# Kernel optimization log

Hardware: AMD Instinct MI355X
Metric: run time of the kernel (lower is better)

## Reference

```python
import jax, jax.numpy as jnp
import numpy as np

B, H, W, C = 16, 56, 56, 384
HEADS, WIN, SHIFT = 12, 7, 3
HD = C // HEADS
HIDDEN = 4 * C
NWH, NWW = H // WIN, W // WIN
NW = NWH * NWW
WA = WIN * WIN  # 49 tokens per window


def _rel_pos_index():
    coords = np.stack(np.meshgrid(np.arange(WIN), np.arange(WIN), indexing='ij')).reshape(2, -1)
    rel = coords[:, :, None] - coords[:, None, :]          # [2, WA, WA]
    rel = rel.transpose(1, 2, 0)
    rel[:, :, 0] += WIN - 1
    rel[:, :, 1] += WIN - 1
    rel[:, :, 0] *= 2 * WIN - 1
    return rel.sum(-1)                                      # [WA, WA]


def _attn_mask():
    img = np.zeros((H, W))
    cnt = 0
    for hs in (slice(0, -WIN), slice(-WIN, -SHIFT), slice(-SHIFT, None)):
        for ws in (slice(0, -WIN), slice(-WIN, -SHIFT), slice(-SHIFT, None)):
            img[hs, ws] = cnt
            cnt += 1
    mw = img.reshape(NWH, WIN, NWW, WIN).transpose(0, 2, 1, 3).reshape(NW, WA)
    diff = mw[:, None, :] - mw[:, :, None]
    return np.where(diff != 0, -100.0, 0.0).astype(np.float32)  # [NW, WA, WA]


REL_IDX = jnp.asarray(_rel_pos_index())
MASK = jnp.asarray(_attn_mask())


def _ln(x, g, b):
    m = x.mean(-1, keepdims=True)
    v = ((x - m) ** 2).mean(-1, keepdims=True)
    return (x - m) / jnp.sqrt(v + 1e-5) * g + b


def setup_inputs() -> dict:
    key = jax.random.key(0)
    ks = jax.random.split(key, 6)
    s = 0.02
    return {
        'x': jax.random.normal(ks[0], (B, H, W, C), jnp.float32),
        'norm1_g': jnp.ones((C,), jnp.float32),
        'norm1_b': jnp.zeros((C,), jnp.float32),
        'qkv_w': jax.random.normal(ks[1], (C, 3 * C), jnp.float32) * s,
        'qkv_b': jnp.zeros((3 * C,), jnp.float32),
        'rel_bias': jax.random.normal(ks[2], ((2 * WIN - 1) ** 2, HEADS), jnp.float32) * s,
        'proj_w': jax.random.normal(ks[3], (C, C), jnp.float32) * s,
        'proj_b': jnp.zeros((C,), jnp.float32),
        'norm2_g': jnp.ones((C,), jnp.float32),
        'norm2_b': jnp.zeros((C,), jnp.float32),
        'fc1_w': jax.random.normal(ks[4], (C, HIDDEN), jnp.float32) * s,
        'fc1_b': jnp.zeros((HIDDEN,), jnp.float32),
        'fc2_w': jax.random.normal(ks[5], (HIDDEN, C), jnp.float32) * s,
        'fc2_b': jnp.zeros((C,), jnp.float32),
    }


def reference(x, norm1_g, norm1_b, qkv_w, qkv_b, rel_bias, proj_w, proj_b,
              norm2_g, norm2_b, fc1_w, fc1_b, fc2_w, fc2_b):
    # ---- shifted-window attention branch ----
    xs = _ln(x, norm1_g, norm1_b)
    xs = jnp.roll(xs, (-SHIFT, -SHIFT), axis=(1, 2))
    # window partition: [B,H,W,C] -> [B*NW, WA, C]
    xw = xs.reshape(B, NWH, WIN, NWW, WIN, C).transpose(0, 1, 3, 2, 4, 5).reshape(B * NW, WA, C)
    qkv = (xw @ qkv_w + qkv_b).reshape(B * NW, WA, 3, HEADS, HD)
    q = qkv[:, :, 0].transpose(0, 2, 1, 3)  # [bw, heads, WA, HD]
    k = qkv[:, :, 1].transpose(0, 2, 1, 3)
    v = qkv[:, :, 2].transpose(0, 2, 1, 3)
    attn = jnp.einsum('bhqd,bhkd->bhqk', q, k) * (HD ** -0.5)
    bias = rel_bias[REL_IDX].transpose(2, 0, 1)  # [heads, WA, WA]
    attn = attn + bias[None]
    attn = attn.reshape(B, NW, HEADS, WA, WA) + MASK[None, :, None]
    attn = jax.nn.softmax(attn, axis=-1).reshape(B * NW, HEADS, WA, WA)
    out = jnp.einsum('bhqk,bhkd->bhqd', attn, v).transpose(0, 2, 1, 3).reshape(B * NW, WA, C)
    out = out @ proj_w + proj_b
    # window reverse + unshift
    out = out.reshape(B, NWH, NWW, WIN, WIN, C).transpose(0, 1, 3, 2, 4, 5).reshape(B, H, W, C)
    out = jnp.roll(out, (SHIFT, SHIFT), axis=(1, 2))
    x = x + out
    # ---- MLP branch ----
    xf = x.reshape(B, H * W, C)
    h = _ln(xf, norm2_g, norm2_b)
    h = jax.nn.gelu(h @ fc1_w + fc1_b, approximate=False)
    xf = xf + (h @ fc2_w + fc2_b)
    return xf.reshape(B, H, W, C)
```

## Files before the change

### kernel.cpp

```cpp
#include <hip/hip_runtime.h>
#include <hip/hip_bf16.h>
#include <math.h>

#define NBATCH 16
#define NW 64
#define WA 49
#define NTOK (NBATCH*NW*WA)
#define CCH 384
#define HIDDEN 1536

typedef __attribute__((ext_vector_type(8))) short short8;
typedef __attribute__((ext_vector_type(4))) float floatx4;

static __device__ __forceinline__ short f2bf(float f){
  unsigned u = __float_as_uint(f);
  unsigned r = (u + 0x7fff + ((u>>16)&1)) >> 16;
  return (short)r;
}

static __device__ __forceinline__ void gload16(const void* g, void* l){
  __builtin_amdgcn_global_load_lds(
      (const __attribute__((address_space(1))) void*)g,
      (__attribute__((address_space(3))) void*)l, 16, 0, 0);
}

static __device__ __forceinline__ long ds_read_b64s(unsigned addr){
  long r;
  asm volatile("ds_read_b64 %0, %1" : "=v"(r) : "v"(addr));
  return r;
}

template<int N> __device__ __forceinline__ void waitvm();
template<> __device__ __forceinline__ void waitvm<0>(){ asm volatile("s_waitcnt vmcnt(0)" ::: "memory"); }
template<> __device__ __forceinline__ void waitvm<5>(){ asm volatile("s_waitcnt vmcnt(5)" ::: "memory"); }

static __device__ __forceinline__ int tok2pix(int t){
  int b = t / (NW*WA);
  int rem = t % (NW*WA);
  int w = rem / WA, a = rem % WA;
  int hs = (w>>3)*7 + a/7;
  int ws = (w&7)*7 + a%7;
  int hp = hs + 3; if (hp >= 56) hp -= 56;
  int wp = ws + 3; if (wp >= 56) wp -= 56;
  return (b*56 + hp)*56 + wp;
}

__global__ void wtconv8(const float* __restrict__ W, unsigned char* __restrict__ Wt, int K, int N){
  int i = blockIdx.x*256 + threadIdx.x;
  if (i >= K*N) return;
  int k = i / N, n = i % N;
  unsigned pk = (unsigned)__builtin_amdgcn_cvt_pk_fp8_f32(W[i], W[i], 0, false);
  Wt[(size_t)n*K + k] = (unsigned char)(pk & 0xff);
}

__global__ void rbt(const float* __restrict__ rb, float* __restrict__ rbT){
  int i = blockIdx.x*256 + threadIdx.x;
  if (i >= 169*12) return;
  int t = i / 12, h = i % 12;
  rbT[h*169 + t] = rb[i];
}

template<int MAP>
__global__ __launch_bounds__(256) void ln_fp8(const float* __restrict__ x,
    const float* __restrict__ g, const float* __restrict__ bta, unsigned char* __restrict__ out){
  int wid = threadIdx.x>>6, lane = threadIdx.x&63;
  int t = blockIdx.x*4 + wid;
  const float* row = x + (size_t)(MAP ? tok2pix(t) : t)*CCH;
  float v[8]; float s=0.f, ss=0.f;
  if (lane < 48){
    float4 p0 = *(const float4*)&row[lane*8];
    float4 p1 = *(const float4*)&row[lane*8+4];
    v[0]=p0.x;v[1]=p0.y;v[2]=p0.z;v[3]=p0.w;
    v[4]=p1.x;v[5]=p1.y;v[6]=p1.z;v[7]=p1.w;
    #pragma unroll
    for (int i=0;i<8;i++){ s+=v[i]; ss+=v[i]*v[i]; }
  }
  #pragma unroll
  for (int off=32; off; off>>=1){ s += __shfl_xor(s,off); ss += __shfl_xor(ss,off); }
  float mean = s*(1.f/384.f);
  float var  = ss*(1.f/384.f) - mean*mean;
  float inv  = rsqrtf(var + 1e-5f);
  if (lane < 48){
    float4 g0 = *(const float4*)&g[lane*8],  g1 = *(const float4*)&g[lane*8+4];
    float4 b0 = *(const float4*)&bta[lane*8],b1 = *(const float4*)&bta[lane*8+4];
    float o[8];
    o[0]=(v[0]-mean)*inv*g0.x+b0.x; o[1]=(v[1]-mean)*inv*g0.y+b0.y;
    o[2]=(v[2]-mean)*inv*g0.z+b0.z; o[3]=(v[3]-mean)*inv*g0.w+b0.w;
    o[4]=(v[4]-mean)*inv*g1.x+b1.x; o[5]=(v[5]-mean)*inv*g1.y+b1.y;
    o[6]=(v[6]-mean)*inv*g1.z+b1.z; o[7]=(v[7]-mean)*inv*g1.w+b1.w;
    unsigned w0 = (unsigned)__builtin_amdgcn_cvt_pk_fp8_f32(o[0], o[1], 0, false);
    w0 = (unsigned)__builtin_amdgcn_cvt_pk_fp8_f32(o[2], o[3], (int)w0, true);
    unsigned w1 = (unsigned)__builtin_amdgcn_cvt_pk_fp8_f32(o[4], o[5], 0, false);
    w1 = (unsigned)__builtin_amdgcn_cvt_pk_fp8_f32(o[6], o[7], (int)w1, true);
    uint2 pk; pk.x = w0; pk.y = w1;
    *(uint2*)&out[(size_t)t*CCH + lane*8] = pk;
  }
}

template<int EPI, int KK>
__global__ __launch_bounds__(512) void gemmF8(const unsigned char* __restrict__ A8,
    const unsigned char* __restrict__ B8, const float* __restrict__ bias,
    const float* __restrict__ res, void* __restrict__ outp,
    int N, int gx)
{
  __shared__ unsigned char As8[2][256][128];
  __shared__ unsigned char Bs8[2][64][128];
  const int tid = threadIdx.x, lane = tid & 63, wid = tid >> 6;
  const int fr = lane & 15, fg = lane >> 4;
  const int wm = wid >> 1, wn = wid & 1;

  const int nwg = gridDim.x;
  const int q = nwg >> 3, r = nwg & 7;
  const int xcd = blockIdx.x & 7, pos = blockIdx.x >> 3;
  const int wgid = (xcd < r ? xcd*(q+1) : r*(q+1) + (xcd-r)*q) + pos;
  const int m0 = (wgid / gx) * 256, n0 = (wgid % gx) * 64;

  floatx4 acc[4][2];
  #pragma unroll
  for (int m=0;m<4;m++)
    #pragma unroll
    for (int n=0;n<2;n++) acc[m][n] = (floatx4){0.f,0.f,0.f,0.f};

  const int srow = tid >> 3;
  const int scolb = ((tid & 7) ^ (srow & 7)) * 16;
  const unsigned char* gA = A8 + (size_t)(m0 + srow) * KK + scolb;
  const unsigned char* gB = B8 + (size_t)(n0 + srow) * KK + scolb;
  constexpr int a64 = 64 * KK;
  unsigned char* aB = &As8[0][wid*8][0];
  unsigned char* bB = &Bs8[0][wid*8][0];
  constexpr int nt = KK >> 7;

  const unsigned aLds = (unsigned)(uintptr_t)&As8[0][0][0];
  const unsigned bLds = (unsigned)(uintptr_t)&Bs8[0][0][0];
  const unsigned rowOffA = (unsigned)((wm*64 + fr)*128);
  const unsigned rowOffB = (unsigned)((wn*32 + fr)*128);
  unsigned pcc[4];
  #pragma unroll
  for (int kk=0;kk<4;kk++)
    pcc[kk] = (unsigned)((((kk*2 + (fg>>1)) ^ (fr&7))*16) + (fg&1)*8);

#define STAGE8(tt, bb) do{                                            \
    const int k0_ = (tt) << 7;                                        \
    unsigned char* a_ = aB + (bb)*256*128;                            \
    unsigned char* b_ = bB + (bb)*64*128;                             \
    gload16(gA + k0_,          a_);                                   \
    gload16(gA + k0_ +   a64,  a_ +  8192);                           \
    gload16(gA + k0_ + 2*a64,  a_ + 16384);                           \
    gload16(gA + k0_ + 3*a64,  a_ + 24576);                           \
    gload16(gB + k0_,          b_);                                   \
  }while(0)

  STAGE8(0, 0);
  #pragma unroll
  for (int t = 0; t < nt; ++t){
    const int buf = t & 1;
    if (t + 1 < nt){
      STAGE8(t+1, buf^1);
      waitvm<5>();
    } else {
      waitvm<0>();
    }
    __builtin_amdgcn_s_barrier();
    const unsigned aoff = aLds + (unsigned)buf*32768u + rowOffA;
    const unsigned boff = bLds + (unsigned)buf*8192u  + rowOffB;
    #pragma unroll
    for (int kk=0; kk<4; ++kk){
      const unsigned pc = pcc[kk];
      long af[4], bq[2];
      #pragma unroll
      for (int m=0;m<4;m++) af[m] = ds_read_b64s(aoff + (unsigned)(m*2048) + pc);
      #pragma unroll
      for (int n=0;n<2;n++) bq[n] = ds_read_b64s(boff + (unsigned)(n*2048) + pc);
      asm volatile("s_waitcnt lgkmcnt(0)" ::: "memory");
      __builtin_amdgcn_sched_barrier(0);
      __builtin_amdgcn_s_setprio(1);
      #pragma unroll
      for (int m=0;m<4;m++)
        #pragma unroll
        for (int n=0;n<2;n++)
          acc[m][n] = __builtin_amdgcn_mfma_f32_16x16x32_fp8_fp8(af[m], bq[n], acc[m][n], 0,0,0);
      __builtin_amdgcn_s_setprio(0);
    }
    __builtin_amdgcn_s_barrier();
  }
#undef STAGE8

  __syncthreads();
  if (EPI==2 || EPI==4){
    unsigned char* Cl = (unsigned char*)&As8[0][0][0];
    const float qscale = (EPI==4 && n0 < 384) ? 0.17677669529663687f : 1.f;
    #pragma unroll
    for (int n=0;n<2;n++){
      int col = wn*32 + n*16 + fr;
      float bv = bias[n0 + col];
      #pragma unroll
      for (int m=0;m<4;m++){
        #pragma unroll
        for (int i=0;i<4;i++){
          int row = wm*64 + m*16 + fg*4 + i;
          float v = acc[m][n][i] + bv;
          if (EPI==2){
            float e2 = __expf(-1.702f*v);
            v = v * __builtin_amdgcn_rcpf(1.f + e2);
          } else {
            v *= qscale;
          }
          unsigned pk = (unsigned)__builtin_amdgcn_cvt_pk_fp8_f32(v, v, 0, false);
          Cl[row*64 + col] = (unsigned char)(pk & 0xff);
        }
      }
    }
    __syncthreads();
    const int rr = tid >> 2, slot = tid & 3;
    #pragma unroll
    for (int it=0; it<2; ++it){
      int row = it*128 + rr;
      short8 v = *(const short8*)&Cl[row*64 + slot*16];
      *(short8*)&((unsigned char*)outp)[(size_t)(m0+row)*N + n0 + slot*16] = v;
    }
  } else {
    float* Cl = (float*)&As8[0][0][0];
    #pragma unroll
    for (int n=0;n<2;n++){
      int col = wn*32 + n*16 + fr;
      float bv = bias[n0 + col];
      #pragma unroll
      for (int m=0;m<4;m++){
        #pragma unroll
        for (int i=0;i<4;i++){
          int row = wm*64 + m*16 + fg*4 + i;
          Cl[row*64 + col] = acc[m][n][i] + bv;
        }
      }
    }
    __syncthreads();
    const int rr = tid >> 4, slot = tid & 15;
    #pragma unroll
    for (int it=0; it<8; ++it){
      int row = it*32 + rr;
      float4 v = *(const float4*)&Cl[row*64 + slot*4];
      size_t idx;
      if (EPI==5){
        int p = tok2pix(m0+row);
        idx = (size_t)p*CCH + n0 + slot*4;
      } else {
        idx = (size_t)(m0+row)*CCH + n0 + slot*4;
      }
      float4 rv = *(const float4*)&res[idx];
      v.x += rv.x; v.y += rv.y; v.z += rv.z; v.w += rv.w;
      *(float4*)&((float*)outp)[idx] = v;
    }
  }
}

__global__ __launch_bounds__(256) void attn_mfma8(const unsigned char* __restrict__ qkv8,
    const float* __restrict__ rbT, unsigned char* __restrict__ att8)
{
  __shared__ unsigned char Pl[4][64][72];
  __shared__ unsigned char Vt[4][32][72];
  __shared__ float lb[4][169];
  __shared__ int grp[64];
  const int wi = blockIdx.x;
  const int wid = threadIdx.x>>6, lane = threadIdx.x&63;
  const int fr = lane&15, fg = lane>>4;
  const int w = wi & 63, wh = w>>3, ww = w&7;
  if (threadIdx.x < 64){
    int t = threadIdx.x;
    int gv = 0;
    if (t < 49){
      int ai = t/7, aj = t%7;
      int hs = wh*7+ai, ws = ww*7+aj;
      int gh = hs<49?0:(hs<53?1:2);
      int gw = ws<49?0:(ws<53?1:2);
      gv = gh*3+gw;
    } else gv = -1;
    grp[t] = gv;
  }
  for (int t = lane; t < 288; t += 64)
    ((long*)&Vt[wid][0][0])[t] = 0;
  __syncthreads();
  const size_t tbase = (size_t)wi*49;

  for (int hi=0; hi<3; ++hi){
    const int h = hi*4 + wid;
    for (int t = lane; t < 169; t += 64) lb[wid][t] = rbT[h*169 + t];
    for (int t = lane; t < 196; t += 64){
      int j = t>>2, d0 = (t&3)*8;
      unsigned long vv = *(const unsigned long*)&qkv8[(tbase+j)*1152 + 768 + h*32 + d0];
      #pragma unroll
      for (int s=0;s<8;s++) Vt[wid][d0+s][j] = (unsigned char)(vv >> (8*s));
    }
    long aq[4], bk[4];
    #pragma unroll
    for (int m=0;m<4;m++){
      int r = m*16+fr;
      aq[m] = (r<49) ? *(const long*)&qkv8[(tbase+r)*1152       + h*32 + fg*8] : 0L;
      bk[m] = (r<49) ? *(const long*)&qkv8[(tbase+r)*1152 + 384 + h*32 + fg*8] : 0L;
    }

    floatx4 sc[4][4];
    #pragma unroll
    for (int m=0;m<4;m++)
      #pragma unroll
      for (int n=0;n<4;n++)
        sc[m][n] = __builtin_amdgcn_mfma_f32_16x16x32_fp8_fp8(aq[m], bk[n], (floatx4){0.f,0.f,0.f,0.f}, 0,0,0);

    int ciC[4], cjC[4], gC[4], cvC[4];
    #pragma unroll
    for (int n=0;n<4;n++){
      int c = n*16+fr;
      ciC[n] = c/7; cjC[n] = c - ciC[n]*7;
      gC[n] = grp[c]; cvC[n] = (c<49);
    }
    #pragma unroll
    for (int m=0;m<4;m++){
      #pragma unroll
      for (int i=0;i<4;i++){
        int r = m*16 + fg*4 + i;
        int rv = (r<49);
        int ri = r/7, rj = r - ri*7;
        int gr = grp[r];
        float mxv = -3e30f;
        #pragma unroll
        for (int n=0;n<4;n++){
          float s;
          if (rv && cvC[n]){
            int dr = ri - ciC[n] + 6, dc = rj - cjC[n] + 6;
            s = sc[m][n][i] + lb[wid][dr*13+dc];
            if (gr != gC[n]) s -= 100.f;
          } else s = -3e30f;
          sc[m][n][i] = s;
          mxv = fmaxf(mxv, s);
        }
        #pragma unroll
        for (int off=1;off<16;off<<=1) mxv = fmaxf(mxv, __shfl_xor(mxv, off));
        float sum = 0.f;
        #pragma unroll
        for (int n=0;n<4;n++){
          float e = __expf(sc[m][n][i]-mxv);
          sc[m][n][i] = e; sum += e;
        }
        #pragma unroll
        for (int off=1;off<16;off<<=1) sum += __shfl_xor(sum, off);
        float inv = 1.f/sum;
        #pragma unroll
        for (int n=0;n<4;n++){
          float p = sc[m][n][i]*inv;
          unsigned pk = (unsigned)__builtin_amdgcn_cvt_pk_fp8_f32(p, p, 0, false);
          Pl[wid][r][n*16+fr] = (unsigned char)(pk & 0xff);
        }
      }
    }

    long pa[4][2], vb[2][2];
    #pragma unroll
    for (int m=0;m<4;m++)
      #pragma unroll
      for (int ks=0;ks<2;ks++)
        pa[m][ks] = *(const long*)&Pl[wid][m*16+fr][ks*32+fg*8];
    #pragma unroll
    for (int n2=0;n2<2;n2++)
      #pragma unroll
      for (int ks=0;ks<2;ks++)
        vb[n2][ks] = *(const long*)&Vt[wid][n2*16+fr][ks*32+fg*8];
    floatx4 oc[4][2];
    #pragma unroll
    for (int m=0;m<4;m++)
      #pragma unroll
      for (int n2=0;n2<2;n2++){
        oc[m][n2] = (floatx4){0.f,0.f,0.f,0.f};
        #pragma unroll
        for (int ks=0;ks<2;ks++)
          oc[m][n2] = __builtin_amdgcn_mfma_f32_16x16x32_fp8_fp8(pa[m][ks], vb[n2][ks], oc[m][n2], 0,0,0);
      }
    #pragma unroll
    for (int m=0;m<4;m++){
      #pragma unroll
      for (int i=0;i<4;i++){
        int r = m*16 + fg*4 + i;
        if (r < 49){
          #pragma unroll
          for (int n2=0;n2<2;n2++){
            float v = oc[m][n2][i];
            unsigned pk = (unsigned)__builtin_amdgcn_cvt_pk_fp8_f32(v, v, 0, false);
            att8[(tbase+r)*384 + h*32 + n2*16 + fr] = (unsigned char)(pk & 0xff);
          }
        }
      }
    }
  }
}

extern "C" void kernel_launch(void* const* d_in, const int* in_sizes, int n_in,
                              void* d_out, int out_size, void* d_ws, size_t ws_size,
                              hipStream_t stream)
{
  const float* x      = (const float*)d_in[0];
  const float* n1g    = (const float*)d_in[1];
  const float* n1b    = (const float*)d_in[2];
  const float* qkv_w  = (const float*)d_in[3];
  const float* qkv_b  = (const float*)d_in[4];
  const float* relb   = (const float*)d_in[5];
  const float* proj_w = (const float*)d_in[6];
  const float* proj_b = (const float*)d_in[7];
  const float* n2g    = (const float*)d_in[8];
  const float* n2b    = (const float*)d_in[9];
  const float* fc1_w  = (const float*)d_in[10];
  const float* fc1_b  = (const float*)d_in[11];
  const float* fc2_w  = (const float*)d_in[12];
  const float* fc2_b  = (const float*)d_in[13];

  char* ws = (char*)d_ws;
  const size_t SZ_XW  = (size_t)NTOK*CCH*2;
  const size_t SZ_QKV = (size_t)NTOK*1152*2;
  const size_t SZ_ATT = SZ_XW;
  const size_t SZ_Y   = (size_t)NTOK*CCH*4;

  unsigned char* xw8  = (unsigned char*)(ws);
  unsigned char* qkv8 = (unsigned char*)(ws + SZ_XW);
  unsigned char* att8 = (unsigned char*)(ws + SZ_XW + SZ_QKV);
  float* y     = (float*)(ws + SZ_XW + SZ_QKV + SZ_ATT);
  char*  wbuf  = ws + SZ_XW + SZ_QKV + SZ_ATT + SZ_Y;
  unsigned char* qkvW8 = (unsigned char*)wbuf;
  unsigned char* projW8= qkvW8 + (size_t)1152*384;
  unsigned char* fc1W8 = projW8 + (size_t)384*384;
  unsigned char* fc2W8 = fc1W8 + (size_t)1536*384;
  float* rbT           = (float*)(fc2W8 + (size_t)384*1536);
  unsigned char* hbuf8 = qkv8;
  unsigned char* hin8  = xw8;

  wtconv8<<<dim3((384*1152+255)/256), dim3(256), 0, stream>>>(qkv_w, qkvW8, 384, 1152);
  wtconv8<<<dim3((384*384 +255)/256), dim3(256), 0, stream>>>(proj_w, projW8, 384, 384);
  wtconv8<<<dim3((384*1536+255)/256), dim3(256), 0, stream>>>(fc1_w, fc1W8, 384, 1536);
  wtconv8<<<dim3((1536*384+255)/256), dim3(256), 0, stream>>>(fc2_w, fc2W8, 1536, 384);
  rbt<<<dim3((169*12+255)/256), dim3(256), 0, stream>>>(relb, rbT);

  ln_fp8<1><<<dim3(NTOK/4), dim3(256), 0, stream>>>(x, n1g, n1b, xw8);
  gemmF8<4,384><<<dim3(18*196), dim3(512), 0, stream>>>(xw8, qkvW8, qkv_b, nullptr, qkv8, 1152, 18);
  attn_mfma8<<<dim3(NBATCH*NW), dim3(256), 0, stream>>>(qkv8, rbT, att8);
  gemmF8<5,384><<<dim3(6*196),  dim3(512), 0, stream>>>(att8, projW8, proj_b, x, y, 384, 6);
  ln_fp8<0><<<dim3(NTOK/4), dim3(256), 0, stream>>>(y, n2g, n2b, hin8);
  gemmF8<2,384><<<dim3(24*196), dim3(512), 0, stream>>>(hin8, fc1W8, fc1_b, nullptr, hbuf8, 1536, 24);
  gemmF8<3,1536><<<dim3(6*196), dim3(512), 0, stream>>>(hbuf8, fc2W8, fc2_b, y, (float*)d_out, 384, 6);
}
```

Measured before the change: 333.2 us.

## Add A-stationary GEMM for K=384 layers and store residual stream in bf16

Adds a new gemmA kernel that loads a 128-row fp8 A tile (full K=384) into LDS once and loops over all N chunks, with the B fragments read straight from global memory into registers and double-buffered. It replaces the tiled gemmF8 for the QKV, proj and fc1 GEMMs, launching a persistent-style grid of 392 workgroups so A is not re-read for every N tile. The intermediate residual y is now stored as bf16 instead of fp32, which halves its write and read traffic in proj, LN2 and fc2. The cost is lower precision on the residual stream and B reads that are not staged through LDS, which may be less efficient.

```diff
diff --git a/kernel.cpp b/kernel.cpp
--- a/kernel.cpp
+++ b/kernel.cpp
@@ -16,6 +16,9 @@
   unsigned u = __float_as_uint(f);
   unsigned r = (u + 0x7fff + ((u>>16)&1)) >> 16;
   return (short)r;
+}
+static __device__ __forceinline__ float bf2f(short s){
+  return __uint_as_float(((unsigned)(unsigned short)s)<<16);
 }
 
 static __device__ __forceinline__ void gload16(const void* g, void* l){
@@ -60,18 +63,26 @@
   rbT[h*169 + t] = rb[i];
 }
 
-template<int MAP>
-__global__ __launch_bounds__(256) void ln_fp8(const float* __restrict__ x,
+template<int MAP, int BF>
+__global__ __launch_bounds__(256) void ln_fp8(const void* __restrict__ xv,
     const float* __restrict__ g, const float* __restrict__ bta, unsigned char* __restrict__ out){
   int wid = threadIdx.x>>6, lane = threadIdx.x&63;
   int t = blockIdx.x*4 + wid;
-  const float* row = x + (size_t)(MAP ? tok2pix(t) : t)*CCH;
+  const size_t roff = (size_t)(MAP ? tok2pix(t) : t)*CCH;
   float v[8]; float s=0.f, ss=0.f;
   if (lane < 48){
-    float4 p0 = *(const float4*)&row[lane*8];
-    float4 p1 = *(const float4*)&row[lane*8+4];
-    v[0]=p0.x;v[1]=p0.y;v[2]=p0.z;v[3]=p0.w;
-    v[4]=p1.x;v[5]=p1.y;v[6]=p1.z;v[7]=p1.w;
+    if (BF){
+      const short* row = (const short*)xv + roff;
+      short8 p = *(const short8*)&row[lane*8];
+      #pragma unroll
+      for (int i=0;i<8;i++) v[i] = bf2f(p[i]);
+    } else {
+      const float* row = (const float*)xv + roff;
+      float4 p0 = *(const float4*)&row[lane*8];
+      float4 p1 = *(const float4*)&row[lane*8+4];
+      v[0]=p0.x;v[1]=p0.y;v[2]=p0.z;v[3]=p0.w;
+      v[4]=p1.x;v[5]=p1.y;v[6]=p1.z;v[7]=p1.w;
+    }
     #pragma unroll
     for (int i=0;i<8;i++){ s+=v[i]; ss+=v[i]*v[i]; }
   }
@@ -97,10 +108,174 @@
   }
 }
 
+template<int EPI, int NCH>
+__global__ __launch_bounds__(256) void gemmA(const unsigned char* __restrict__ A8,
+    const unsigned char* __restrict__ B8, const float* __restrict__ bias,
+    const void* __restrict__ resv, void* __restrict__ outp, int N)
+{
+  __shared__ unsigned char Al[3][128][128];
+  __shared__ long Clbuf[2048];
+  const int tid = threadIdx.x, lane = tid & 63, wid = tid >> 6;
+  const int fr = lane & 15, fg = lane >> 4;
+  const int wm = wid >> 1, wn = wid & 1;
+
+  const int nwg = gridDim.x;
+  const int q = nwg >> 3;
+  const int xcd = blockIdx.x & 7, pos = blockIdx.x >> 3;
+  const int wgid = xcd*q + pos;
+  const int m0 = wgid * 128;
+
+  const int srow = tid >> 3;
+  const int scolb = ((tid & 7) ^ (srow & 7)) * 16;
+  {
+    unsigned char* aB = &Al[0][wid*8][0];
+    #pragma unroll
+    for (int c=0;c<3;c++)
+      #pragma unroll
+      for (int j=0;j<4;j++)
+        gload16(A8 + (size_t)(m0 + srow + 32*j)*384 + c*128 + scolb,
+                aB + c*16384 + j*4096);
+  }
+  waitvm<0>();
+  __builtin_amdgcn_s_barrier();
+
+  const unsigned aLds = (unsigned)(uintptr_t)&Al[0][0][0];
+  const unsigned rowOffA = (unsigned)((wm*64 + fr)*128);
+  unsigned pcc[4];
+  #pragma unroll
+  for (int kk=0;kk<4;kk++)
+    pcc[kk] = (unsigned)((((kk*2 + (fg>>1)) ^ (fr&7))*16) + (fg&1)*8);
+
+  floatx4 acc[4][2];
+  long bqA[3][4][2], bqB[3][4][2];
+
+#define LOADB(BQ, ncv) do{                                                     \
+    const unsigned char* Bp0 = B8 + (size_t)((ncv)*64 + wn*32 + fr)*384 + fg*8;\
+    const unsigned char* Bp1 = Bp0 + 16*384;                                   \
+    _Pragma("unroll")                                                          \
+    for (int t_=0;t_<3;t_++)                                                   \
+      _Pragma("unroll")                                                        \
+      for (int kk_=0;kk_<4;kk_++){                                             \
+        BQ[t_][kk_][0] = *(const long*)(Bp0 + t_*128 + kk_*32);                \
+        BQ[t_][kk_][1] = *(const long*)(Bp1 + t_*128 + kk_*32);                \
+      }                                                                        \
+  }while(0)
+
+#define ZACC do{                                                               \
+    _Pragma("unroll")                                                          \
+    for (int m_=0;m_<4;m_++){ acc[m_][0]=(floatx4){0.f,0.f,0.f,0.f};           \
+                              acc[m_][1]=(floatx4){0.f,0.f,0.f,0.f}; }         \
+  }while(0)
+
+#define COMPUTE(BQ) do{                                                        \
+    _Pragma("unroll")                                                          \
+    for (int t_=0;t_<3;t_++)                                                   \
+      _Pragma("unroll")                                                        \
+      for (int kk_=0;kk_<4;kk_++){                                             \
+        long af_[4];                                                           \
+        _Pragma("unroll")                                                      \
+        for (int m_=0;m_<4;m_++)                                               \
+          af_[m_] = ds_read_b64s(aLds + (unsigned)(t_*16384) + rowOffA +       \
+                                 (unsigned)(m_*2048) + pcc[kk_]);              \
+        asm volatile("s_waitcnt lgkmcnt(0)" ::: "memory");                     \
+        __builtin_amdgcn_sched_barrier(0);                                     \
+        __builtin_amdgcn_s_setprio(1);                                         \
+        _Pragma("unroll")                                                      \
+        for (int m_=0;m_<4;m_++){                                              \
+          acc[m_][0] = __builtin_amdgcn_mfma_f32_16x16x32_fp8_fp8(af_[m_], BQ[t_][kk_][0], acc[m_][0], 0,0,0); \
+          acc[m_][1] = __builtin_amdgcn_mfma_f32_16x16x32_fp8_fp8(af_[m_], BQ[t_][kk_][1], acc[m_][1], 0,0,0); \
+        }                                                                      \
+        __builtin_amdgcn_s_setprio(0);                                         \
+      }                                                                        \
+  }while(0)
+
+#define EPILOG(ncv) do{                                                        \
+    asm volatile("s_waitcnt lgkmcnt(0)" ::: "memory");                         \
+    __builtin_amdgcn_s_barrier();             \
+    if constexpr (EPI==2 || EPI==4){                                           \
+      unsigned char* C8 = (unsigned char*)Clbuf;                               \
+      const float qs = (EPI==4 && (ncv) < 6) ? 0.17677669529663687f : 1.f;     \
+      _Pragma("unroll")                                                        \
+      for (int n_=0;n_<2;n_++){                                                \
+        int col = wn*32 + n_*16 + fr;                                          \
+        float bv = bias[(ncv)*64 + col];                                       \
+        _Pragma("unroll")                                                      \
+        for (int m_=0;m_<4;m_++)                                               \
+          _Pragma("unroll")                                                    \
+          for (int i_=0;i_<4;i_++){                                            \
+            int row = wm*64 + m_*16 + fg*4 + i_;                               \
+            float v_ = acc[m_][n_][i_] + bv;                                   \
+            if (EPI==2){                                                       \
+              float e2 = __expf(-1.702f*v_);                                   \
+              v_ = v_ * __builtin_amdgcn_rcpf(1.f + e2);                       \
+            } else v_ *= qs;                                                   \
+            unsigned pk_ = (unsigned)__builtin_amdgcn_cvt_pk_fp8_f32(v_, v_, 0, false); \
+            C8[row*64 + col] = (unsigned char)(pk_ & 0xff);                    \
+          }                                                                    \
+      }                                                                        \
+      asm volatile("s_waitcnt lgkmcnt(0)" ::: "memory");                       \
+      __builtin_amdgcn_s_barrier();                                            \
+      const int rr_ = tid >> 2, sl_ = tid & 3;                                 \
+      _Pragma("unroll")                                                        \
+      for (int it_=0;it_<2;it_++){                                             \
+        int row = it_*64 + rr_;                                                \
+        short8 v_ = *(const short8*)&C8[row*64 + sl_*16];                      \
+        *(short8*)&((unsigned char*)outp)[(size_t)(m0+row)*N + (ncv)*64 + sl_*16] = v_; \
+      }                                                                        \
+    } else {                                                                   \
+      short* Cs = (short*)Clbuf;                                               \
+      const float* res = (const float*)resv;                                   \
+      _Pragma("unroll")                                                        \
+      for (int n_=0;n_<2;n_++){                                                \
+        int col = wn*32 + n_*16 + fr;                                          \
+        float bv = bias[(ncv)*64 + col];                                       \
+        _Pragma("unroll")                                                      \
+        for (int m_=0;m_<4;m_++)                                               \
+          _Pragma("unroll")                                                    \
+          for (int i_=0;i_<4;i_++){                                            \
+            int row = wm*64 + m_*16 + fg*4 + i_;                               \
+            Cs[row*64 + col] = f2bf(acc[m_][n_][i_] + bv);                     \
+          }                                                                    \
+      }                                                                        \
+      asm volatile("s_waitcnt lgkmcnt(0)" ::: "memory");                       \
+      __builtin_amdgcn_s_barrier();                                            \
+      const int rr_ = tid >> 3, sl_ = tid & 7;                                 \
+      _Pragma("unroll")                                                        \
+      for (int it_=0;it_<4;it_++){                                             \
+        int row = it_*32 + rr_;                                                \
+        short8 v_ = *(const short8*)&Cs[row*64 + sl_*8];                       \
+        int p_ = tok2pix(m0+row);                                              \
+        size_t base = (size_t)p_*CCH + (ncv)*64 + sl_*8;                       \
+        float4 x0 = *(const float4*)&res[base];                                \
+        float4 x1 = *(const float4*)&res[base+4];                              \
+        short8 o_;                                                             \
+        o_[0]=f2bf(x0.x+bf2f(v_[0])); o_[1]=f2bf(x0.y+bf2f(v_[1]));            \
+        o_[2]=f2bf(x0.z+bf2f(v_[2])); o_[3]=f2bf(x0.w+bf2f(v_[3]));            \
+        o_[4]=f2bf(x1.x+bf2f(v_[4])); o_[5]=f2bf(x1.y+bf2f(v_[5]));            \
+        o_[6]=f2bf(x1.z+bf2f(v_[6])); o_[7]=f2bf(x1.w+bf2f(v_[7]));            \
+        *(short8*)&((short*)outp)[base] = o_;                                  \
+      }                                                                        \
+    }                                                                          \
+  }while(0)
+
+  LOADB(bqA, 0);
+  for (int i2=0; i2<NCH/2; ++i2){
+    const int ncA = 2*i2, ncB = 2*i2+1;
+    LOADB(bqB, ncB);
+    ZACC; COMPUTE(bqA); EPILOG(ncA);
+    if (ncA+2 < NCH) LOADB(bqA, ncA+2);
+    ZACC; COMPUTE(bqB); EPILOG(ncB);
+  }
+#undef LOADB
+#undef ZACC
+#undef COMPUTE
+#undef EPILOG
+}
+
 template<int EPI, int KK>
 __global__ __launch_bounds__(512) void gemmF8(const unsigned char* __restrict__ A8,
     const unsigned char* __restrict__ B8, const float* __restrict__ bias,
-    const float* __restrict__ res, void* __restrict__ outp,
+    const void* __restrict__ resv, void* __restrict__ outp,
     int N, int gx)
 {
   __shared__ unsigned char As8[2][256][128];
@@ -186,70 +361,31 @@
 #undef STAGE8
 
   __syncthreads();
-  if (EPI==2 || EPI==4){
-    unsigned char* Cl = (unsigned char*)&As8[0][0][0];
-    const float qscale = (EPI==4 && n0 < 384) ? 0.17677669529663687f : 1.f;
-    #pragma unroll
-    for (int n=0;n<2;n++){
-      int col = wn*32 + n*16 + fr;
-      float bv = bias[n0 + col];
-      #pragma unroll
-      for (int m=0;m<4;m++){
-        #pragma unroll
-        for (int i=0;i<4;i++){
-          int row = wm*64 + m*16 + fg*4 + i;
-          float v = acc[m][n][i] + bv;
-          if (EPI==2){
-            float e2 = __expf(-1.702f*v);
-            v = v * __builtin_amdgcn_rcpf(1.f + e2);
-          } else {
-            v *= qscale;
-          }
-          unsigned pk = (unsigned)__builtin_amdgcn_cvt_pk_fp8_f32(v, v, 0, false);
-          Cl[row*64 + col] = (unsigned char)(pk & 0xff);
-        }
+  const short* resb = (const short*)resv;
+  float* Cl = (float*)&As8[0][0][0];
+  #pragma unroll
+  for (int n=0;n<2;n++){
+    int col = wn*32 + n*16 + fr;
+    float bv = bias[n0 + col];
+    #pragma unroll
+    for (int m=0;m<4;m++){
+      #pragma unroll
+      for (int i=0;i<4;i++){
+        int row = wm*64 + m*16 + fg*4 + i;
+        Cl[row*64 + col] = acc[m][n][i] + bv;
       }
     }
-    __syncthreads();
-    const int rr = tid >> 2, slot = tid & 3;
-    #pragma unroll
-    for (int it=0; it<2; ++it){
-      int row = it*128 + rr;
-      short8 v = *(const short8*)&Cl[row*64 + slot*16];
-      *(short8*)&((unsigned char*)outp)[(size_t)(m0+row)*N + n0 + slot*16] = v;
-    }
-  } else {
-    float* Cl = (float*)&As8[0][0][0];
-    #pragma unroll
-    for (int n=0;n<2;n++){
-      int col = wn*32 + n*16 + fr;
-      float bv = bias[n0 + col];
-      #pragma unroll
-      for (int m=0;m<4;m++){
-        #pragma unroll
-        for (int i=0;i<4;i++){
-          int row = wm*64 + m*16 + fg*4 + i;
-          Cl[row*64 + col] = acc[m][n][i] + bv;
-        }
-      }
-    }
-    __syncthreads();
-    const int rr = tid >> 4, slot = tid & 15;
-    #pragma unroll
-    for (int it=0; it<8; ++it){
-      int row = it*32 + rr;
-      float4 v = *(const float4*)&Cl[row*64 + slot*4];
-      size_t idx;
-      if (EPI==5){
-        int p = tok2pix(m0+row);
-        idx = (size_t)p*CCH + n0 + slot*4;
-      } else {
-        idx = (size_t)(m0+row)*CCH + n0 + slot*4;
-      }
-      float4 rv = *(const float4*)&res[idx];
-      v.x += rv.x; v.y += rv.y; v.z += rv.z; v.w += rv.w;
-      *(float4*)&((float*)outp)[idx] = v;
-    }
+  }
+  __syncthreads();
+  const int rr = tid >> 4, slot = tid & 15;
+  #pragma unroll
+  for (int it=0; it<8; ++it){
+    int row = it*32 + rr;
+    float4 v = *(const float4*)&Cl[row*64 + slot*4];
+    size_t idx = (size_t)(m0+row)*CCH + n0 + slot*4;
+    short4 rv = *(const short4*)&resb[idx];
+    v.x += bf2f(rv.x); v.y += bf2f(rv.y); v.z += bf2f(rv.z); v.w += bf2f(rv.w);
+    *(float4*)&((float*)outp)[idx] = v;
   }
 }
 
@@ -419,7 +555,7 @@
   unsigned char* xw8  = (unsigned char*)(ws);
   unsigned char* qkv8 = (unsigned char*)(ws + SZ_XW);
   unsigned char* att8 = (unsigned char*)(ws + SZ_XW + SZ_QKV);
-  float* y     = (float*)(ws + SZ_XW + SZ_QKV + SZ_ATT);
+  short* y     = (short*)(ws + SZ_XW + SZ_QKV + SZ_ATT);
   char*  wbuf  = ws + SZ_XW + SZ_QKV + SZ_ATT + SZ_Y;
   unsigned char* qkvW8 = (unsigned char*)wbuf;
   unsigned char* projW8= qkvW8 + (size_t)1152*384;
@@ -435,11 +571,11 @@
   wtconv8<<<dim3((1536*384+255)/256), dim3(256), 0, stream>>>(fc2_w, fc2W8, 1536, 384);
   rbt<<<dim3((169*12+255)/256), dim3(256), 0, stream>>>(relb, rbT);
 
-  ln_fp8<1><<<dim3(NTOK/4), dim3(256), 0, stream>>>(x, n1g, n1b, xw8);
-  gemmF8<4,384><<<dim3(18*196), dim3(512), 0, stream>>>(xw8, qkvW8, qkv_b, nullptr, qkv8, 1152, 18);
+  ln_fp8<1,0><<<dim3(NTOK/4), dim3(256), 0, stream>>>(x, n1g, n1b, xw8);
+  gemmA<4,18><<<dim3(392), dim3(256), 0, stream>>>(xw8, qkvW8, qkv_b, nullptr, qkv8, 1152);
   attn_mfma8<<<dim3(NBATCH*NW), dim3(256), 0, stream>>>(qkv8, rbT, att8);
-  gemmF8<5,384><<<dim3(6*196),  dim3(512), 0, stream>>>(att8, projW8, proj_b, x, y, 384, 6);
-  ln_fp8<0><<<dim3(NTOK/4), dim3(256), 0, stream>>>(y, n2g, n2b, hin8);
-  gemmF8<2,384><<<dim3(24*196), dim3(512), 0, stream>>>(hin8, fc1W8, fc1_b, nullptr, hbuf8, 1536, 24);
+  gemmA<5,6><<<dim3(392), dim3(256), 0, stream>>>(att8, projW8, proj_b, x, y, 384);
+  ln_fp8<0,1><<<dim3(NTOK/4), dim3(256), 0, stream>>>(y, n2g, n2b, hin8);
+  gemmA<2,24><<<dim3(392), dim3(256), 0, stream>>>(hin8, fc1W8, fc1_b, nullptr, hbuf8, 1536);
   gemmF8<3,1536><<<dim3(6*196), dim3(512), 0, stream>>>(hbuf8, fc2W8, fc2_b, y, (float*)d_out, 384, 6);
 }
```

After: 527.5 us. 58.3% more time.
